# Kernel optimization log

Hardware: AMD Instinct MI355X
Metric: run time of the kernel (lower is better)

The kernel has to match this reference:

```python
import math
import jax, jax.numpy as jnp
import numpy as np

B, T, D = 2048, 50, 256
NEG = -100000.0

def setup_inputs() -> dict:
    key = jax.random.key(0)
    ks = jax.random.split(key, 9)
    return {
        "x": jax.random.normal(ks[0], (B, T, D), dtype=jnp.float32),
        "mask": jax.random.randint(ks[1], (B, T, 1), 0, 2, dtype=jnp.int32),
        "time_decay": jax.random.uniform(ks[2], (B, T, 1), dtype=jnp.float32),
        "Wq": jax.random.normal(ks[3], (D, D), dtype=jnp.float32) * (1.0 / math.sqrt(D)),
        "bq": jax.random.normal(ks[4], (D,), dtype=jnp.float32) * 0.01,
        "Wk": jax.random.normal(ks[5], (D, D), dtype=jnp.float32) * (1.0 / math.sqrt(D)),
        "bk": jax.random.normal(ks[6], (D,), dtype=jnp.float32) * 0.01,
        "Wv": jax.random.normal(ks[7], (D, D), dtype=jnp.float32) * (1.0 / math.sqrt(D)),
        "bv": jax.random.normal(ks[8], (D,), dtype=jnp.float32) * 0.01,
    }

def reference(x, mask, time_decay, Wq, bq, Wk, bk, Wv, bv):
    # PositionalEncoding.forward: elementwise multiply by time-decay (broadcast over d_model)
    x = x * time_decay  # [B,T,D]
    q = jnp.einsum('btd,ed->bte', x, Wq) + bq
    k = jnp.einsum('btd,ed->bte', x, Wk) + bk
    v = jnp.einsum('btd,ed->bte', x, Wv) + bv
    # unusual Q/K-side masking (masked_fill before the matmul)
    keep = mask != 0  # [B,T,1]
    q = jnp.where(keep, q, NEG)
    k = jnp.where(keep, k, NEG)
    score = jnp.einsum('btd,bsd->bts', q, k) / math.sqrt(D)  # [B,T,T]
    score = jax.nn.softmax(score, axis=-1)
    # dropout is identity in eval mode
    out = jnp.einsum('bts,bsd->btd', score, v)  # [B,T,D]
    return out[:, -1, :]  # [B,D]
```

## Files before the change

kernel.cpp:

```cpp
#include <hip/hip_runtime.h>


namespace {
constexpr int kB = 2048;
constexpr int kT = 50;
constexpr int kD = 256;
constexpr double kNeg = -100000.0;
constexpr int oM2 = 0;
constexpr int oWvp = 65536;
constexpr int oV0 = 131072;
constexpr int oC = 131328;
constexpr int oW1 = 131584;
constexpr int oW2 = 131840;
constexpr int oDbl = 132096;
}

__global__ __launch_bounds__(256) void precomp(
    const float* __restrict__ Wq, const float* __restrict__ bq,
    const float* __restrict__ Wk, const float* __restrict__ bk,
    const float* __restrict__ Wv, float* __restrict__ ws) {
  const int t = threadIdx.x;
  const int wave = t >> 6;
  const int lane = t & 63;
  const int blk = blockIdx.x;
  __shared__ float coefL[kD];
  __shared__ double red[3][4];

  if (blk < 256) {
    const int a = blk;
    coefL[t] = Wq[(size_t)t * kD + a];
    __syncthreads();
    const float* kcol = Wk + t;
    float pre[8];
#pragma unroll
    for (int k = 0; k < 8; ++k) pre[k] = kcol[(size_t)k * kD];
    float acc = 0.f;
    for (int j0 = 0; j0 < kD; j0 += 8) {
      float cur[8];
#pragma unroll
      for (int k = 0; k < 8; ++k) cur[k] = pre[k];
      const int nx = (j0 + 8 < kD) ? (j0 + 8) : 0;
#pragma unroll
      for (int k = 0; k < 8; ++k) pre[k] = kcol[(size_t)(nx + k) * kD];
#pragma unroll
      for (int k = 0; k < 8; ++k) acc += coefL[j0 + k] * cur[k];
    }
    ws[oM2 + (a >> 2) * 1024 + 4 * t + (a & 3)] = acc;
  } else if (blk < 258) {
    const float* W = (blk == 256) ? Wk : Wq;
    const float* coef = (blk == 256) ? bq : bk;
    coefL[t] = coef[t];
    __syncthreads();
    const float* col = W + t;
    float pre[8];
#pragma unroll
    for (int k = 0; k < 8; ++k) pre[k] = col[(size_t)k * kD];
    double a0 = 0.0, a1 = 0.0;
    for (int j0 = 0; j0 < kD; j0 += 8) {
      float cur[8];
#pragma unroll
      for (int k = 0; k < 8; ++k) cur[k] = pre[k];
      const int nx = (j0 + 8 < kD) ? (j0 + 8) : 0;
#pragma unroll
      for (int k = 0; k < 8; ++k) pre[k] = col[(size_t)(nx + k) * kD];
#pragma unroll
      for (int k = 0; k < 8; ++k) {
        const double w = (double)cur[k];
        a0 += (double)coefL[j0 + k] * w;
        a1 += w;
      }
    }
    if (blk == 256) {
      ws[oV0 + t] = (float)a0;
      ws[oC + t] = (float)a1;
    } else {
      ws[oW1 + t] = (float)a0;
      ws[oW2 + t] = (float)a1;
      double p0 = (double)bk[t];
      double p1 = (double)bq[t] * (double)bk[t];
      double p2 = (double)bq[t];
#pragma unroll
      for (int off = 32; off; off >>= 1) {
        p0 += __shfl_xor(p0, off);
        p1 += __shfl_xor(p1, off);
        p2 += __shfl_xor(p2, off);
      }
      if (lane == 0) {
        red[0][wave] = p0;
        red[1][wave] = p1;
        red[2][wave] = p2;
      }
      __syncthreads();
      if (t == 0) {
        double* dcw = (double*)(ws + oDbl);
        dcw[0] = red[0][0] + red[0][1] + red[0][2] + red[0][3];
        dcw[1] = red[1][0] + red[1][1] + red[1][2] + red[1][3];
        dcw[2] = red[2][0] + red[2][1] + red[2][2] + red[2][3];
      }
    }
  } else {
    const int d4b = (blk - 258) * 4;
    float4 in[4];
#pragma unroll
    for (int k = 0; k < 4; ++k)
      in[k] = *(const float4*)(Wv + (size_t)t * kD + 4 * (d4b + k));
    float4* Wvp = (float4*)(ws + oWvp);
#pragma unroll
    for (int k = 0; k < 4; ++k) Wvp[(size_t)(d4b + k) * kD + t] = in[k];
  }
}

__global__ __launch_bounds__(512) void ukernel(
    const float* __restrict__ x, const float* __restrict__ td,
    const float* __restrict__ ws, float* __restrict__ uout) {
  const int tid = threadIdx.x;
  const int lane = tid & 63;
  const int w = tid >> 6;
  const int b0 = blockIdx.x * 4;
  __shared__ __align__(16) float xsL[4][kD];
  __shared__ __align__(16) float scr[2][4][kD];
  const float4* M2v = (const float4*)(ws + oM2);

  if (w < 4) {
    const int b = b0 + w;
    const float tdl = td[(size_t)b * kT + kT - 1];
    const float4 xv =
        ((const float4*)(x + ((size_t)b * kT + kT - 1) * kD))[lane];
    float4 xs;
    xs.x = xv.x * tdl; xs.y = xv.y * tdl;
    xs.z = xv.z * tdl; xs.w = xv.w * tdl;
    *(float4*)(&xsL[w][4 * lane]) = xs;
  }
  __syncthreads();

  {
    const int gU = w & 3;
    const int kh = w >> 2;
    const int col = 64 * gU + lane;
    const int kb = kh * 32;
    float4 A = M2v[(size_t)(kb + 0) * 256 + col];
    float4 B = M2v[(size_t)(kb + 1) * 256 + col];
    float4 C = M2v[(size_t)(kb + 2) * 256 + col];
    float4 D = M2v[(size_t)(kb + 3) * 256 + col];
    float acc[4] = {0.f, 0.f, 0.f, 0.f};
    for (int k4 = kb; k4 < kb + 32; k4 += 2) {
      const float4 c0 = A, c1 = B;
      A = C;
      B = D;
      const int n0 = (k4 + 4 < kb + 32) ? k4 + 4 : kb;
      const int n1 = (k4 + 5 < kb + 32) ? k4 + 5 : kb;
      C = M2v[(size_t)n0 * 256 + col];
      D = M2v[(size_t)n1 * 256 + col];
#pragma unroll
      for (int jb = 0; jb < 4; ++jb) {
        const float4 x0 = *(const float4*)(&xsL[jb][4 * k4]);
        const float4 x1 = *(const float4*)(&xsL[jb][4 * (k4 + 1)]);
        acc[jb] += x0.x * c0.x + x0.y * c0.y + x0.z * c0.z + x0.w * c0.w +
                   x1.x * c1.x + x1.y * c1.y + x1.z * c1.z + x1.w * c1.w;
      }
    }
#pragma unroll
    for (int jb = 0; jb < 4; ++jb) scr[kh][jb][col] = acc[jb];
  }
  __syncthreads();

#pragma unroll
  for (int rr = 0; rr < 2; ++rr) {
    const int idx = tid + rr * 512;
    const int mj = idx >> 8;
    const int mcol = idx & 255;
    uout[(size_t)(b0 + mj) * kD + mcol] =
        scr[0][mj][mcol] + scr[1][mj][mcol] + ws[oV0 + mcol];
  }
}

__global__ __launch_bounds__(256) void attnk(
    const float* __restrict__ x, const int* __restrict__ mask,
    const float* __restrict__ td, const float* __restrict__ ws,
    float* __restrict__ uy) {
  const int tid = threadIdx.x;
  const int lane = tid & 63;
  const int q = tid >> 6;
  const int b = blockIdx.x;
  __shared__ __align__(16) float ypart[4][kD];
  __shared__ double mpart[4];
  __shared__ float lpart[4];

  const double* dc = (const double*)(ws + oDbl);

  const float mtd = (lane < kT) ? td[(size_t)b * kT + lane] : 0.f;
  const int mmk = (lane < kT) ? mask[(size_t)b * kT + lane] : 0;
  const float4 c4 = ((const float4*)(ws + oC))[lane];
  const float4 u4 = ((const float4*)(uy + (size_t)b * kD))[lane];

  const float tdl = __shfl(mtd, kT - 1);
  const float4 a1 = ((const float4*)(ws + oW1))[lane];
  const float4 a2 = ((const float4*)(ws + oW2))[lane];
  const float4 xv = ((const float4*)(x + ((size_t)b * kT + kT - 1) * kD))[lane];
  double s1 = (double)xv.x * a1.x + (double)xv.y * a1.y +
              (double)xv.z * a1.z + (double)xv.w * a1.w;
  double s2 = (double)xv.x * a2.x + (double)xv.y * a2.y +
              (double)xv.z * a2.z + (double)xv.w * a2.w;
#pragma unroll
  for (int off = 32; off; off >>= 1) {
    s1 += __shfl_xor(s1, off);
    s2 += __shfl_xor(s2, off);
  }
  const double Qb = (double)tdl * s1 + dc[1];
  const double Sq = (double)tdl * s2 + dc[2];
  const int mqg = __shfl(mmk, kT - 1);
  const float4 v4 = mqg ? u4 : c4;
  const double Cm = kNeg * Sq * 0.0625;
  const double sbkd = dc[0];
  const double Cbb = 256.0 * 1.0e10 * 0.0625;

  const int sbeg = (q == 0) ? 0 : (q == 1) ? 13 : (q == 2) ? 26 : 38;
  const int send = (q == 0) ? 13 : (q == 1) ? 26 : (q == 2) ? 38 : 50;

  const float4* xrow = (const float4*)(x + (size_t)b * kT * kD);
  double m = -1.0e300;
  float l = 0.f;
  float4 y = {0.f, 0.f, 0.f, 0.f};

  const int i0 = (sbeg + 0 < kT) ? sbeg + 0 : kT - 1;
  const int i1 = (sbeg + 1 < kT) ? sbeg + 1 : kT - 1;
  const int i2 = (sbeg + 2 < kT) ? sbeg + 2 : kT - 1;
  const int i3 = (sbeg + 3 < kT) ? sbeg + 3 : kT - 1;
  float4 n0 = xrow[(size_t)i0 * 64 + lane];
  float4 n1 = xrow[(size_t)i1 * 64 + lane];
  float4 n2 = xrow[(size_t)i2 * 64 + lane];
  float4 n3 = xrow[(size_t)i3 * 64 + lane];
  for (int s = sbeg; s < send; s += 4) {
    const float4 r0 = n0, r1 = n1, r2 = n2, r3 = n3;
    {
      const int p0 = (s + 4 < kT) ? s + 4 : kT - 1;
      const int p1 = (s + 5 < kT) ? s + 5 : kT - 1;
      const int p2 = (s + 6 < kT) ? s + 6 : kT - 1;
      const int p3 = (s + 7 < kT) ? s + 7 : kT - 1;
      n0 = xrow[(size_t)p0 * 64 + lane];
      n1 = xrow[(size_t)p1 * 64 + lane];
      n2 = xrow[(size_t)p2 * 64 + lane];
      n3 = xrow[(size_t)p3 * 64 + lane];
    }
    const int s1i = s + 1, s2i = s + 2, s3i = s + 3;
    const int cc0 = s;
    const int cc1 = (s1i < kT) ? s1i : kT - 1;
    const int cc2 = (s2i < kT) ? s2i : kT - 1;
    const int cc3 = (s3i < kT) ? s3i : kT - 1;
    const float tv0 = __shfl(mtd, cc0);
    const float tv1 = __shfl(mtd, cc1);
    const float tv2 = __shfl(mtd, cc2);
    const float tv3 = __shfl(mtd, cc3);
    float4 a0, aa1, a2v, a3;
    a0.x = r0.x * tv0; a0.y = r0.y * tv0; a0.z = r0.z * tv0; a0.w = r0.w * tv0;
    aa1.x = r1.x * tv1; aa1.y = r1.y * tv1; aa1.z = r1.z * tv1; aa1.w = r1.w * tv1;
    a2v.x = r2.x * tv2; a2v.y = r2.y * tv2; a2v.z = r2.z * tv2; a2v.w = r2.w * tv2;
    a3.x = r3.x * tv3; a3.y = r3.y * tv3; a3.z = r3.z * tv3; a3.w = r3.w * tv3;
    float p0 = a0.x * v4.x + a0.y * v4.y + a0.z * v4.z + a0.w * v4.w;
    float p1 = aa1.x * v4.x + aa1.y * v4.y + aa1.z * v4.z + aa1.w * v4.w;
    float p2 = a2v.x * v4.x + a2v.y * v4.y + a2v.z * v4.z + a2v.w * v4.w;
    float p3 = a3.x * v4.x + a3.y * v4.y + a3.z * v4.z + a3.w * v4.w;
#pragma unroll
    for (int off = 32; off; off >>= 1) {
      p0 += __shfl_xor(p0, off);
      p1 += __shfl_xor(p1, off);
      p2 += __shfl_xor(p2, off);
      p3 += __shfl_xor(p3, off);
    }
    const int ms0 = __shfl(mmk, cc0);
    const int ms1 = __shfl(mmk, cc1);
    const int ms2 = __shfl(mmk, cc2);
    const int ms3 = __shfl(mmk, cc3);
    double sc0, sc1, sc2, sc3;
    if (mqg) {
      sc0 = ms0 ? ((double)p0 + Qb) * 0.0625 : Cm;
      sc1 = ms1 ? ((double)p1 + Qb) * 0.0625 : Cm;
      sc2 = ms2 ? ((double)p2 + Qb) * 0.0625 : Cm;
      sc3 = ms3 ? ((double)p3 + Qb) * 0.0625 : Cm;
    } else {
      sc0 = ms0 ? kNeg * ((double)p0 + sbkd) * 0.0625 : Cbb;
      sc1 = ms1 ? kNeg * ((double)p1 + sbkd) * 0.0625 : Cbb;
      sc2 = ms2 ? kNeg * ((double)p2 + sbkd) * 0.0625 : Cbb;
      sc3 = ms3 ? kNeg * ((double)p3 + sbkd) * 0.0625 : Cbb;
    }
    if (s1i >= send) sc1 = -1.0e300;
    if (s2i >= send) sc2 = -1.0e300;
    if (s3i >= send) sc3 = -1.0e300;
    double mnew = m;
    if (sc0 > mnew) mnew = sc0;
    if (sc1 > mnew) mnew = sc1;
    if (sc2 > mnew) mnew = sc2;
    if (sc3 > mnew) mnew = sc3;
    const float al = __expf((float)(m - mnew));
    const float e0 = __expf((float)(sc0 - mnew));
    const float e1 = __expf((float)(sc1 - mnew));
    const float e2 = __expf((float)(sc2 - mnew));
    const float e3 = __expf((float)(sc3 - mnew));
    m = mnew;
    l = l * al + e0 + e1 + e2 + e3;
    y.x = y.x * al + e0 * a0.x + e1 * aa1.x + e2 * a2v.x + e3 * a3.x;
    y.y = y.y * al + e0 * a0.y + e1 * aa1.y + e2 * a2v.y + e3 * a3.y;
    y.z = y.z * al + e0 * a0.z + e1 * aa1.z + e2 * a2v.z + e3 * a3.z;
    y.w = y.w * al + e0 * a0.w + e1 * aa1.w + e2 * a2v.w + e3 * a3.w;
  }
  if (lane == 0) {
    mpart[q] = m;
    lpart[q] = l;
  }
  *(float4*)(&ypart[q][4 * lane]) = y;
  __syncthreads();

  {
    const int d = tid;
    double M = mpart[0];
    if (mpart[1] > M) M = mpart[1];
    if (mpart[2] > M) M = mpart[2];
    if (mpart[3] > M) M = mpart[3];
    const float e0 = __expf((float)(mpart[0] - M));
    const float e1 = __expf((float)(mpart[1] - M));
    const float e2 = __expf((float)(mpart[2] - M));
    const float e3 = __expf((float)(mpart[3] - M));
    const float lsum = lpart[0] * e0 + lpart[1] * e1 + lpart[2] * e2 +
                       lpart[3] * e3;
    const float inv = 1.0f / lsum;
    uy[(size_t)b * kD + d] =
        (ypart[0][d] * e0 + ypart[1][d] * e1 + ypart[2][d] * e2 +
         ypart[3][d] * e3) *
        inv;
  }
}

__global__ __launch_bounds__(512) void okernel(
    const float* __restrict__ bv, const float* __restrict__ ws,
    float* __restrict__ io) {
  const int tid = threadIdx.x;
  const int lane = tid & 63;
  const int w = tid >> 6;
  const int b0 = blockIdx.x * 4;
  __shared__ __align__(16) float yL[4][kD];
  __shared__ __align__(16) float scr[2][4][kD];
  const float4* Wvv = (const float4*)(ws + oWvp);

#pragma unroll
  for (int rr = 0; rr < 2; ++rr) {
    const int idx = tid + rr * 512;
    const int mj = idx >> 8;
    const int mcol = idx & 255;
    yL[mj][mcol] = io[(size_t)(b0 + mj) * kD + mcol];
  }
  __syncthreads();

  {
    const int gU = w & 3;
    const int kh = w >> 2;
    const int col = 64 * gU + lane;
    const int kb = kh * 32;
    float4 A = Wvv[(size_t)(kb + 0) * 256 + col];
    float4 B = Wvv[(size_t)(kb + 1) * 256 + col];
    float4 C = Wvv[(size_t)(kb + 2) * 256 + col];
    float4 D = Wvv[(size_t)(kb + 3) * 256 + col];
    float acc[4] = {0.f, 0.f, 0.f, 0.f};
    for (int k4 = kb; k4 < kb + 32; k4 += 2) {
      const float4 c0 = A, c1 = B;
      A = C;
      B = D;
      const int n0 = (k4 + 4 < kb + 32) ? k4 + 4 : kb;
      const int n1 = (k4 + 5 < kb + 32) ? k4 + 5 : kb;
      C = Wvv[(size_t)n0 * 256 + col];
      D = Wvv[(size_t)n1 * 256 + col];
#pragma unroll
      for (int jb = 0; jb < 4; ++jb) {
        const float4 y0 = *(const float4*)(&yL[jb][4 * k4]);
        const float4 y1 = *(const float4*)(&yL[jb][4 * (k4 + 1)]);
        acc[jb] += y0.x * c0.x + y0.y * c0.y + y0.z * c0.z + y0.w * c0.w +
                   y1.x * c1.x + y1.y * c1.y + y1.z * c1.z + y1.w * c1.w;
      }
    }
#pragma unroll
    for (int jb = 0; jb < 4; ++jb) scr[kh][jb][col] = acc[jb];
  }
  __syncthreads();

#pragma unroll
  for (int rr = 0; rr < 2; ++rr) {
    const int idx = tid + rr * 512;
    const int mj = idx >> 8;
    const int mcol = idx & 255;
    io[(size_t)(b0 + mj) * kD + mcol] =
        scr[0][mj][mcol] + scr[1][mj][mcol] + bv[mcol];
  }
}

extern "C" void kernel_launch(void* const* d_in, const int* in_sizes, int n_in,
                              void* d_out, int out_size, void* d_ws,
                              size_t ws_size, hipStream_t stream) {
  const float* x = (const float*)d_in[0];
  const int* mask = (const int*)d_in[1];
  const float* td = (const float*)d_in[2];
  const float* Wq = (const float*)d_in[3];
  const float* bq = (const float*)d_in[4];
  const float* Wk = (const float*)d_in[5];
  const float* bk = (const float*)d_in[6];
  const float* Wv = (const float*)d_in[7];
  const float* bv = (const float*)d_in[8];
  float* ws = (float*)d_ws;
  float* out = (float*)d_out;
  (void)in_sizes; (void)n_in; (void)out_size; (void)ws_size;

  hipLaunchKernelGGL(precomp, dim3(274), dim3(256), 0, stream, Wq, bq, Wk, bk,
                     Wv, ws);
  hipLaunchKernelGGL(ukernel, dim3(kB / 4), dim3(512), 0, stream, x, td,
                     (const float*)ws, out);
  hipLaunchKernelGGL(attnk, dim3(kB), dim3(256), 0, stream, x, mask, td,
                     (const float*)ws, out);
  hipLaunchKernelGGL(okernel, dim3(kB / 4), dim3(512), 0, stream, bv,
                     (const float*)ws, out);
}
```

Baseline: 206.0 us.

## Stage x tile in LDS and replace online softmax with two-pass attention

The attention kernel now loads each batch's full 50x256 x tile into padded shared memory. Scores are computed by a lane-per-row partial dot product split across four waves, followed by a single-wave softmax with wave reductions and a per-dimension weighted sum over the staged rows. This removes the per-step shuffle reductions and the serial online-softmax rescaling of the previous streaming loop. In exchange each block needs about 51 KB of LDS, which limits occupancy, and adds several block barriers.

After: 210.9 us. +2.4%, slower.

```diff
diff --git a/kernel.cpp b/kernel.cpp
--- a/kernel.cpp
+++ b/kernel.cpp
@@ -13,6 +13,7 @@
 constexpr int oW1 = 131584;
 constexpr int oW2 = 131840;
 constexpr int oDbl = 132096;
+constexpr int kP = 257;
 }
 
 __global__ __launch_bounds__(256) void precomp(
@@ -180,153 +181,109 @@
     float* __restrict__ uy) {
   const int tid = threadIdx.x;
   const int lane = tid & 63;
-  const int q = tid >> 6;
+  const int w = tid >> 6;
   const int b = blockIdx.x;
-  __shared__ __align__(16) float ypart[4][kD];
-  __shared__ double mpart[4];
-  __shared__ float lpart[4];
-
-  const double* dc = (const double*)(ws + oDbl);
+  __shared__ __align__(16) float xL[kT * kP + 4];
+  __shared__ float vL[kD];
+  __shared__ float pL[4][64];
+  __shared__ float wL[64];
+
+  const float* xb = x + (size_t)b * kT * kD;
+  const int mqg = mask[(size_t)b * kT + (kT - 1)];
+
+  {
+    const float4* xv4 = (const float4*)xb;
+#pragma unroll
+    for (int k = 0; k < 13; ++k) {
+      const int idx4 = tid + 256 * k;
+      if (idx4 < kT * 64) {
+        const int s = idx4 >> 6;
+        const int d4 = idx4 & 63;
+        const float4 v = xv4[idx4];
+        float* dst = &xL[s * kP + 4 * d4];
+        dst[0] = v.x; dst[1] = v.y; dst[2] = v.z; dst[3] = v.w;
+      }
+    }
+    vL[tid] = mqg ? uy[(size_t)b * kD + tid] : ws[oC + tid];
+  }
 
   const float mtd = (lane < kT) ? td[(size_t)b * kT + lane] : 0.f;
   const int mmk = (lane < kT) ? mask[(size_t)b * kT + lane] : 0;
-  const float4 c4 = ((const float4*)(ws + oC))[lane];
-  const float4 u4 = ((const float4*)(uy + (size_t)b * kD))[lane];
-
-  const float tdl = __shfl(mtd, kT - 1);
-  const float4 a1 = ((const float4*)(ws + oW1))[lane];
-  const float4 a2 = ((const float4*)(ws + oW2))[lane];
-  const float4 xv = ((const float4*)(x + ((size_t)b * kT + kT - 1) * kD))[lane];
-  double s1 = (double)xv.x * a1.x + (double)xv.y * a1.y +
-              (double)xv.z * a1.z + (double)xv.w * a1.w;
-  double s2 = (double)xv.x * a2.x + (double)xv.y * a2.y +
-              (double)xv.z * a2.z + (double)xv.w * a2.w;
-#pragma unroll
-  for (int off = 32; off; off >>= 1) {
-    s1 += __shfl_xor(s1, off);
-    s2 += __shfl_xor(s2, off);
-  }
-  const double Qb = (double)tdl * s1 + dc[1];
-  const double Sq = (double)tdl * s2 + dc[2];
-  const int mqg = __shfl(mmk, kT - 1);
-  const float4 v4 = mqg ? u4 : c4;
-  const double Cm = kNeg * Sq * 0.0625;
-  const double sbkd = dc[0];
-  const double Cbb = 256.0 * 1.0e10 * 0.0625;
-
-  const int sbeg = (q == 0) ? 0 : (q == 1) ? 13 : (q == 2) ? 26 : 38;
-  const int send = (q == 0) ? 13 : (q == 1) ? 26 : (q == 2) ? 38 : 50;
-
-  const float4* xrow = (const float4*)(x + (size_t)b * kT * kD);
-  double m = -1.0e300;
-  float l = 0.f;
-  float4 y = {0.f, 0.f, 0.f, 0.f};
-
-  const int i0 = (sbeg + 0 < kT) ? sbeg + 0 : kT - 1;
-  const int i1 = (sbeg + 1 < kT) ? sbeg + 1 : kT - 1;
-  const int i2 = (sbeg + 2 < kT) ? sbeg + 2 : kT - 1;
-  const int i3 = (sbeg + 3 < kT) ? sbeg + 3 : kT - 1;
-  float4 n0 = xrow[(size_t)i0 * 64 + lane];
-  float4 n1 = xrow[(size_t)i1 * 64 + lane];
-  float4 n2 = xrow[(size_t)i2 * 64 + lane];
-  float4 n3 = xrow[(size_t)i3 * 64 + lane];
-  for (int s = sbeg; s < send; s += 4) {
-    const float4 r0 = n0, r1 = n1, r2 = n2, r3 = n3;
-    {
-      const int p0 = (s + 4 < kT) ? s + 4 : kT - 1;
-      const int p1 = (s + 5 < kT) ? s + 5 : kT - 1;
-      const int p2 = (s + 6 < kT) ? s + 6 : kT - 1;
-      const int p3 = (s + 7 < kT) ? s + 7 : kT - 1;
-      n0 = xrow[(size_t)p0 * 64 + lane];
-      n1 = xrow[(size_t)p1 * 64 + lane];
-      n2 = xrow[(size_t)p2 * 64 + lane];
-      n3 = xrow[(size_t)p3 * 64 + lane];
-    }
-    const int s1i = s + 1, s2i = s + 2, s3i = s + 3;
-    const int cc0 = s;
-    const int cc1 = (s1i < kT) ? s1i : kT - 1;
-    const int cc2 = (s2i < kT) ? s2i : kT - 1;
-    const int cc3 = (s3i < kT) ? s3i : kT - 1;
-    const float tv0 = __shfl(mtd, cc0);
-    const float tv1 = __shfl(mtd, cc1);
-    const float tv2 = __shfl(mtd, cc2);
-    const float tv3 = __shfl(mtd, cc3);
-    float4 a0, aa1, a2v, a3;
-    a0.x = r0.x * tv0; a0.y = r0.y * tv0; a0.z = r0.z * tv0; a0.w = r0.w * tv0;
-    aa1.x = r1.x * tv1; aa1.y = r1.y * tv1; aa1.z = r1.z * tv1; aa1.w = r1.w * tv1;
-    a2v.x = r2.x * tv2; a2v.y = r2.y * tv2; a2v.z = r2.z * tv2; a2v.w = r2.w * tv2;
-    a3.x = r3.x * tv3; a3.y = r3.y * tv3; a3.z = r3.z * tv3; a3.w = r3.w * tv3;
-    float p0 = a0.x * v4.x + a0.y * v4.y + a0.z * v4.z + a0.w * v4.w;
-    float p1 = aa1.x * v4.x + aa1.y * v4.y + aa1.z * v4.z + aa1.w * v4.w;
-    float p2 = a2v.x * v4.x + a2v.y * v4.y + a2v.z * v4.z + a2v.w * v4.w;
-    float p3 = a3.x * v4.x + a3.y * v4.y + a3.z * v4.z + a3.w * v4.w;
+
+  double Qb = 0.0, Sq = 0.0;
+  if (w == 0) {
+    const double* dc = (const double*)(ws + oDbl);
+    const float tdl = __shfl(mtd, kT - 1);
+    const float4 a1 = ((const float4*)(ws + oW1))[lane];
+    const float4 a2 = ((const float4*)(ws + oW2))[lane];
+    const float4 xv = ((const float4*)(xb + (size_t)(kT - 1) * kD))[lane];
+    double s1 = (double)xv.x * a1.x + (double)xv.y * a1.y +
+                (double)xv.z * a1.z + (double)xv.w * a1.w;
+    double s2 = (double)xv.x * a2.x + (double)xv.y * a2.y +
+                (double)xv.z * a2.z + (double)xv.w * a2.w;
 #pragma unroll
     for (int off = 32; off; off >>= 1) {
-      p0 += __shfl_xor(p0, off);
-      p1 += __shfl_xor(p1, off);
-      p2 += __shfl_xor(p2, off);
-      p3 += __shfl_xor(p3, off);
-    }
-    const int ms0 = __shfl(mmk, cc0);
-    const int ms1 = __shfl(mmk, cc1);
-    const int ms2 = __shfl(mmk, cc2);
-    const int ms3 = __shfl(mmk, cc3);
-    double sc0, sc1, sc2, sc3;
-    if (mqg) {
-      sc0 = ms0 ? ((double)p0 + Qb) * 0.0625 : Cm;
-      sc1 = ms1 ? ((double)p1 + Qb) * 0.0625 : Cm;
-      sc2 = ms2 ? ((double)p2 + Qb) * 0.0625 : Cm;
-      sc3 = ms3 ? ((double)p3 + Qb) * 0.0625 : Cm;
+      s1 += __shfl_xor(s1, off);
+      s2 += __shfl_xor(s2, off);
+    }
+    Qb = (double)tdl * s1 + dc[1];
+    Sq = (double)tdl * s2 + dc[2];
+  }
+  __syncthreads();
+
+  {
+    const int srow = (lane < kT) ? lane : 0;
+    const float* xrow = &xL[srow * kP];
+    const int dbase = 64 * w;
+    float acc0 = 0.f, acc1 = 0.f;
+#pragma unroll
+    for (int t = 0; t < 64; t += 2) {
+      acc0 += xrow[dbase + t] * vL[dbase + t];
+      acc1 += xrow[dbase + t + 1] * vL[dbase + t + 1];
+    }
+    pL[w][lane] = acc0 + acc1;
+  }
+  __syncthreads();
+
+  if (w == 0) {
+    const double* dc = (const double*)(ws + oDbl);
+    const float praw = pL[0][lane] + pL[1][lane] + pL[2][lane] + pL[3][lane];
+    const float pfull = praw * mtd;
+    const double Cm = kNeg * Sq * 0.0625;
+    const double sbkd = dc[0];
+    const double Cbb = 256.0 * 1.0e10 * 0.0625;
+    double sc;
+    if (lane < kT) {
+      if (mqg)
+        sc = mmk ? ((double)pfull + Qb) * 0.0625 : Cm;
+      else
+        sc = mmk ? kNeg * ((double)pfull + sbkd) * 0.0625 : Cbb;
     } else {
-      sc0 = ms0 ? kNeg * ((double)p0 + sbkd) * 0.0625 : Cbb;
-      sc1 = ms1 ? kNeg * ((double)p1 + sbkd) * 0.0625 : Cbb;
-      sc2 = ms2 ? kNeg * ((double)p2 + sbkd) * 0.0625 : Cbb;
-      sc3 = ms3 ? kNeg * ((double)p3 + sbkd) * 0.0625 : Cbb;
-    }
-    if (s1i >= send) sc1 = -1.0e300;
-    if (s2i >= send) sc2 = -1.0e300;
-    if (s3i >= send) sc3 = -1.0e300;
-    double mnew = m;
-    if (sc0 > mnew) mnew = sc0;
-    if (sc1 > mnew) mnew = sc1;
-    if (sc2 > mnew) mnew = sc2;
-    if (sc3 > mnew) mnew = sc3;
-    const float al = __expf((float)(m - mnew));
-    const float e0 = __expf((float)(sc0 - mnew));
-    const float e1 = __expf((float)(sc1 - mnew));
-    const float e2 = __expf((float)(sc2 - mnew));
-    const float e3 = __expf((float)(sc3 - mnew));
-    m = mnew;
-    l = l * al + e0 + e1 + e2 + e3;
-    y.x = y.x * al + e0 * a0.x + e1 * aa1.x + e2 * a2v.x + e3 * a3.x;
-    y.y = y.y * al + e0 * a0.y + e1 * aa1.y + e2 * a2v.y + e3 * a3.y;
-    y.z = y.z * al + e0 * a0.z + e1 * aa1.z + e2 * a2v.z + e3 * a3.z;
-    y.w = y.w * al + e0 * a0.w + e1 * aa1.w + e2 * a2v.w + e3 * a3.w;
-  }
-  if (lane == 0) {
-    mpart[q] = m;
-    lpart[q] = l;
-  }
-  *(float4*)(&ypart[q][4 * lane]) = y;
+      sc = -1.0e300;
+    }
+    double m = sc;
+#pragma unroll
+    for (int off = 32; off; off >>= 1) {
+      const double o = __shfl_xor(m, off);
+      if (o > m) m = o;
+    }
+    const float e = __expf((float)(sc - m));
+    float l = e;
+#pragma unroll
+    for (int off = 32; off; off >>= 1) l += __shfl_xor(l, off);
+    wL[lane] = e * (1.0f / l) * mtd;
+  }
   __syncthreads();
 
   {
     const int d = tid;
-    double M = mpart[0];
-    if (mpart[1] > M) M = mpart[1];
-    if (mpart[2] > M) M = mpart[2];
-    if (mpart[3] > M) M = mpart[3];
-    const float e0 = __expf((float)(mpart[0] - M));
-    const float e1 = __expf((float)(mpart[1] - M));
-    const float e2 = __expf((float)(mpart[2] - M));
-    const float e3 = __expf((float)(mpart[3] - M));
-    const float lsum = lpart[0] * e0 + lpart[1] * e1 + lpart[2] * e2 +
-                       lpart[3] * e3;
-    const float inv = 1.0f / lsum;
-    uy[(size_t)b * kD + d] =
-        (ypart[0][d] * e0 + ypart[1][d] * e1 + ypart[2][d] * e2 +
-         ypart[3][d] * e3) *
-        inv;
+    float y0 = 0.f, y1 = 0.f;
+#pragma unroll
+    for (int s = 0; s < kT; s += 2) {
+      y0 += wL[s] * xL[s * kP + d];
+      y1 += wL[s + 1] * xL[(s + 1) * kP + d];
+    }
+    uy[(size_t)b * kD + d] = y0 + y1;
   }
 }
 
```
